# Kernel tuning notes

Hardware: AMD Instinct MI355X
Metric: run time of the kernel (lower is better)

The kernel has to match this reference:

```python
import jax, jax.numpy as jnp
import numpy as np

B, T, SD, CD = 2048, 512, 8, 8
H = 64 + SD  # control_rnn_size + state_dim = 72


def setup_inputs() -> dict:
    key = jax.random.key(0)
    ks = jax.random.split(key, 16)
    s = 0.05
    inp = {
        "x": jax.random.normal(ks[0], (B, SD), jnp.float32),
        "rnn_input": jax.random.normal(ks[1], (B, T, CD + 1), jnp.float32),
        "deltas": jax.random.uniform(ks[2], (B, T, 1), jnp.float32),
        "h_lens": jax.random.randint(ks[3], (B,), T // 2, T + 1, jnp.int32),
        "W_ih": s * jax.random.normal(ks[4], (4 * H, CD + 1), jnp.float32),
        "W_hh": s * jax.random.normal(ks[5], (4 * H, H), jnp.float32),
        "b_ih": jnp.zeros((4 * H,), jnp.float32),
        "b_hh": jnp.zeros((4 * H,), jnp.float32),
        "enc_W1": s * jax.random.normal(ks[6], (256, SD), jnp.float32),
        "enc_b1": jnp.zeros((256,), jnp.float32),
        "enc_W2": s * jax.random.normal(ks[7], (256, 256), jnp.float32),
        "enc_b2": jnp.zeros((256,), jnp.float32),
        "enc_W3": s * jax.random.normal(ks[8], (64, 256), jnp.float32),
        "enc_b3": jnp.zeros((64,), jnp.float32),
        "dec_W1": s * jax.random.normal(ks[9], (288, H), jnp.float32),
        "dec_b1": jnp.zeros((288,), jnp.float32),
        "dec_W2": s * jax.random.normal(ks[10], (288, 288), jnp.float32),
        "dec_b2": jnp.zeros((288,), jnp.float32),
        "dec_W3": s * jax.random.normal(ks[11], (SD, 288), jnp.float32),
        "dec_b3": jnp.zeros((SD,), jnp.float32),
    }
    return inp


def _mlp(z, Ws_bs):
    # Linear->Tanh repeated, final Linear without activation
    *hidden, (Wf, bf) = Ws_bs
    for W, b in hidden:
        z = jnp.tanh(z @ W.T + b)
    return z @ Wf.T + bf


def _lstm(rnn_input, h0, c0, W_ih, W_hh, b_ih, b_hh):
    # rnn_input: [B,T,I]; h0,c0: [B,H]. PyTorch gate order: i,f,g,o.
    x_proj = rnn_input @ W_ih.T + (b_ih + b_hh)  # [B,T,4H]

    def step(carry, xt):
        h, c = carry
        gates = xt + h @ W_hh.T
        i, f, g, o = jnp.split(gates, 4, axis=-1)
        i, f, o = jax.nn.sigmoid(i), jax.nn.sigmoid(f), jax.nn.sigmoid(o)
        c = f * c + i * jnp.tanh(g)
        h = o * jnp.tanh(c)
        return (h, c), h

    _, hs = jax.lax.scan(step, (h0, c0), jnp.swapaxes(x_proj, 0, 1))
    return jnp.swapaxes(hs, 0, 1)  # [B,T,H]


def reference(x, rnn_input, deltas, h_lens, W_ih, W_hh, b_ih, b_hh,
              enc_W1, enc_b1, enc_W2, enc_b2, enc_W3, enc_b3,
              dec_W1, dec_b1, dec_W2, dec_b2, dec_W3, dec_b3):
    h0 = _mlp(x, [(enc_W1, enc_b1), (enc_W2, enc_b2), (enc_W3, enc_b3)])  # [B,64]
    h0_stack = jnp.concatenate([x, h0], axis=1)  # [B,H]
    c0 = jnp.zeros_like(h0_stack)
    h = _lstm(rnn_input, h0_stack, c0, W_ih, W_hh, b_ih, b_hh)  # [B,T,H]
    # roll by 1 with h0 in slot 0
    h_shift = jnp.concatenate([h0_stack[:, None, :], h[:, :-1, :]], axis=1)
    encoded = (1.0 - deltas) * h_shift + deltas * h  # [B,T,H]
    dec_in = encoded[jnp.arange(encoded.shape[0]), h_lens - 1, :]  # [B,H]
    out = _mlp(dec_in, [(dec_W1, dec_b1), (dec_W2, dec_b2), (dec_W3, dec_b3)])
    return out[:, :SD]
```

## Files before the change

kernel.cpp:

```cpp
#include <hip/hip_runtime.h>
#include <cstdint>

#define HH 72
#define NR 8
#define NTH 576
#define NBLK 256
#define TT 512

typedef __attribute__((ext_vector_type(8))) _Float16 half8;
typedef __attribute__((ext_vector_type(4))) float f32x4;

#if __has_builtin(__builtin_amdgcn_exp2f)
#define EXP2(x) __builtin_amdgcn_exp2f(x)
#else
#define EXP2(x) exp2f(x)
#endif
#if __has_builtin(__builtin_amdgcn_rcpf)
#define RCP(x) __builtin_amdgcn_rcpf(x)
#else
#define RCP(x) (1.0f/(x))
#endif

__device__ __forceinline__ float fsig(float x) {
  float e = EXP2(x * -1.442695040888963f);
  return RCP(1.0f + e);
}
__device__ __forceinline__ float ftanh(float x) {
  float e = EXP2(x * -2.885390081777927f);
  return fmaf(2.0f, RCP(1.0f + e), -1.0f);
}

__device__ __forceinline__ unsigned short f2h(float v) {
  union { _Float16 h; unsigned short u; } cv;
  cv.h = (_Float16)v;
  return cv.u;
}

__device__ __forceinline__ int bidx(int k, int m) {
  return ((k >> 5)*4 + ((k >> 3) & 3))*64 + m*8 + (k & 7);
}

__device__ __forceinline__ float cellUpd(float ig, float fg, float gg, float og, float& c) {
  c = fmaf(fsig(fg), c, fsig(ig)*ftanh(gg));
  return fsig(og)*ftanh(c);
}

#define FMA4(A, W_, P_) { \
  const float4 _fa = *(const float4*)(P_); \
  A[0] = fmaf((W_), _fa.x, A[0]); A[1] = fmaf((W_), _fa.y, A[1]); \
  A[2] = fmaf((W_), _fa.z, A[2]); A[3] = fmaf((W_), _fa.w, A[3]); }

__global__ void cfm_sort(const int* __restrict__ h_lens, int* __restrict__ perm) {
  __shared__ int hist[257];
  __shared__ int offs[257];
  const int t = threadIdx.x;
  for (int i = t; i < 257; i += 256) hist[i] = 0;
  __syncthreads();
  for (int i = t; i < 2048; i += 256) {
    int bkt = min(max(h_lens[i] - 256, 0), 256);
    atomicAdd(&hist[bkt], 1);
  }
  __syncthreads();
  if (t == 0) { int s = 0; for (int i = 0; i < 257; ++i) { offs[i] = s; s += hist[i]; } }
  __syncthreads();
  for (int i = t; i < 2048; i += 256) {
    int bkt = min(max(h_lens[i] - 256, 0), 256);
    int pos = atomicAdd(&offs[bkt], 1);
    perm[pos] = i;
  }
}

__global__ __launch_bounds__(NTH, 2)
void cfm_main(const float* __restrict__ x, const float* __restrict__ rnn,
              const float* __restrict__ deltas, const int* __restrict__ h_lens,
              const float* __restrict__ W_ih, const float* __restrict__ W_hh,
              const float* __restrict__ b_ih, const float* __restrict__ b_hh,
              const float* __restrict__ eW1, const float* __restrict__ eb1,
              const float* __restrict__ eW2, const float* __restrict__ eb2,
              const float* __restrict__ eW3, const float* __restrict__ eb3,
              const float* __restrict__ dW1, const float* __restrict__ db1,
              const float* __restrict__ dW2, const float* __restrict__ db2,
              const float* __restrict__ dW3, const float* __restrict__ db3,
              const int* __restrict__ perm, float* __restrict__ out)
{
  __shared__ __align__(16) unsigned short hF[2][768];
  __shared__ __align__(16) float gS[2304];
  __shared__ __align__(16) float rnnS[2336];
  __shared__ __align__(16) float snapP[NR][HH];
  __shared__ __align__(16) float snapC[NR][HH];
  __shared__ __align__(16) float hS[HH*NR];
  __shared__ __align__(16) float xS[8*NR];
  __shared__ int brS[NR];
  __shared__ int idxS[NR];
  __shared__ float dS[NR];

  const int t  = threadIdx.x;
  const int bb = blockIdx.x;

  for (int i = t; i < 768; i += NTH) ((unsigned*)hF)[i] = 0;

  if (t < NR) {
    int row = perm ? perm[bb*NR + t] : (bb*NR + t);
    brS[t]  = row;
    idxS[t] = h_lens[row] - 1;
  }
  __syncthreads();

  int maxIdx = idxS[0];
  #pragma unroll
  for (int r = 1; r < NR; ++r) maxIdx = max(maxIdx, idxS[r]);

  const int lane = t & 63;
  const int wv   = t >> 6;
  const int col  = lane & 15;
  const int q_a  = lane >> 4;
  const int cL   = col & 7;
  const int gHi  = col >> 3;
  const int uA   = 4*(2*wv + gHi) + q_a;
  const int cidxE  = idxS[cL];
  const int cidxm1 = cidxE - 1;
  const int ibA  = bidx(uA, cL);
  const int bOff0 = (0*4 + q_a)*64 + cL*8;
  const int bOff1 = (1*4 + q_a)*64 + cL*8;
  const int bOff2 = (2*4 + q_a)*64 + cL*8;
  float cstA = 0.f;

  const int pfR = t / 72;
  const int pfP = t - pfR*72;
  const float4* rnnRow = (const float4*)(rnn + (size_t)brS[pfR]*4608) + pfP;
  float4 pf = rnnRow[0];

  const bool doXt = (t < 72);
  int xtDst = 0, xtSrc = 0;
  if (doXt) {
    int rX = t / 9, kX = t - rX*9;
    xtDst = bidx(72 + kX, rX);
    xtSrc = rX*292 + kX;
  }

  if (t < 64) { int r = t >> 3, k = t & 7; xS[k*8 + r] = x[brS[r]*8 + k]; }
  __syncthreads();

  float* z1S = gS;
  if (t < 512) {
    int n = t >> 1, rh = (t & 1)*4;
    float acc[4];
    float b = eb1[n];
    acc[0]=b; acc[1]=b; acc[2]=b; acc[3]=b;
    #pragma unroll
    for (int k = 0; k < 8; ++k) { float w = eW1[n*8 + k]; FMA4(acc, w, &xS[k*8 + rh]); }
    #pragma unroll
    for (int j = 0; j < 4; ++j) z1S[n*8 + rh + j] = ftanh(acc[j]);
  }
  __syncthreads();
  float* z2S = rnnS;
  if (t < 512) {
    int n = t >> 1, rh = (t & 1)*4;
    float acc[4];
    float b = eb2[n];
    acc[0]=b; acc[1]=b; acc[2]=b; acc[3]=b;
    const float4* w4 = (const float4*)(eW2 + n*256);
    #pragma unroll 4
    for (int k4 = 0; k4 < 64; ++k4) {
      float4 w = w4[k4];
      FMA4(acc, w.x, &z1S[(4*k4+0)*8 + rh]);
      FMA4(acc, w.y, &z1S[(4*k4+1)*8 + rh]);
      FMA4(acc, w.z, &z1S[(4*k4+2)*8 + rh]);
      FMA4(acc, w.w, &z1S[(4*k4+3)*8 + rh]);
    }
    #pragma unroll
    for (int j = 0; j < 4; ++j) z2S[n*8 + rh + j] = ftanh(acc[j]);
  }
  __syncthreads();
  if (t < 128) {
    int o = t >> 1, rh = (t & 1)*4;
    float acc[4];
    float b = eb3[o];
    acc[0]=b; acc[1]=b; acc[2]=b; acc[3]=b;
    const float4* w4 = (const float4*)(eW3 + o*256);
    #pragma unroll 4
    for (int k4 = 0; k4 < 64; ++k4) {
      float4 w = w4[k4];
      FMA4(acc, w.x, &z2S[(4*k4+0)*8 + rh]);
      FMA4(acc, w.y, &z2S[(4*k4+1)*8 + rh]);
      FMA4(acc, w.z, &z2S[(4*k4+2)*8 + rh]);
      FMA4(acc, w.w, &z2S[(4*k4+3)*8 + rh]);
    }
    #pragma unroll
    for (int j = 0; j < 4; ++j) hF[0][bidx(8 + o, rh + j)] = f2h(acc[j]);
  } else if (t < 192) {
    int tt2 = t - 128; int r = tt2 >> 3, k = tt2 & 7;
    hF[0][bidx(k, r)] = f2h(xS[k*8 + r]);
  }

  half8 Af[2][3];
  f32x4 biasq[2];
  #pragma unroll
  for (int i = 0; i < 2; ++i) {
    int u = 4*(2*wv + i) + q_a;
    biasq[i].x = b_ih[u]       + b_hh[u];
    biasq[i].y = b_ih[72 + u]  + b_hh[72 + u];
    biasq[i].z = b_ih[144 + u] + b_hh[144 + u];
    biasq[i].w = b_ih[216 + u] + b_hh[216 + u];
    int nprime = (2*wv + i)*16 + col;
    int srcrow = (nprime & 3)*72 + (nprime >> 2);
    #pragma unroll
    for (int kt = 0; kt < 3; ++kt) {
      union { unsigned short u16[8]; half8 h; } cw;
      #pragma unroll
      for (int j = 0; j < 8; ++j) {
        int k = kt*32 + q_a*8 + j;
        float v = 0.f;
        if (k < 72)      v = W_hh[srcrow*HH + k];
        else if (k < 81) v = W_ih[srcrow*9 + (k - 72)];
        cw.u16[j] = f2h(v);
      }
      Af[i][kt] = cw.h;
    }
  }

#define STEP(PAR) { \
    const unsigned short* hb = &hF[PAR][0]; \
    unsigned short* hn = &hF[(PAR) ^ 1][0]; \
    half8 bf0 = *(const half8*)(hb + bOff0); \
    half8 bf1 = *(const half8*)(hb + bOff1); \
    half8 bf2 = *(const half8*)(hb + bOff2); \
    f32x4 a0 = __builtin_amdgcn_mfma_f32_16x16x32_f16(Af[0][0], bf0, biasq[0], 0, 0, 0); \
    f32x4 a1 = __builtin_amdgcn_mfma_f32_16x16x32_f16(Af[1][0], bf0, biasq[1], 0, 0, 0); \
    a0 = __builtin_amdgcn_mfma_f32_16x16x32_f16(Af[0][1], bf1, a0, 0, 0, 0); \
    a1 = __builtin_amdgcn_mfma_f32_16x16x32_f16(Af[1][1], bf1, a1, 0, 0, 0); \
    a0 = __builtin_amdgcn_mfma_f32_16x16x32_f16(Af[0][2], bf2, a0, 0, 0, 0); \
    a1 = __builtin_amdgcn_mfma_f32_16x16x32_f16(Af[1][2], bf2, a1, 0, 0, 0); \
    float ig = gHi ? a1.x : a0.x; \
    float fg = gHi ? a1.y : a0.y; \
    float gg = gHi ? a1.z : a0.z; \
    float og = gHi ? a1.w : a0.w; \
    float hv = cellUpd(ig, fg, gg, og, cstA); \
    hn[ibA] = f2h(hv); \
    if (step == cidxm1) snapP[cL][uA] = hv; \
    if (step == cidxE)  snapC[cL][uA] = hv; \
    if (doXt && tc < 31) hn[xtDst] = f2h(rnnS[xtSrc + (tc + 1)*9]); \
    __syncthreads(); \
    ++tc; ++step; }

  int step = 0;
  for (int chunk = 0; chunk*32 <= maxIdx; ++chunk) {
    __syncthreads();
    *(float4*)&rnnS[pfR*292 + pfP*4] = pf;
    if ((chunk + 1)*32 <= maxIdx) pf = rnnRow[(chunk + 1)*72];
    __syncthreads();
    if (doXt) hF[0][xtDst] = f2h(rnnS[xtSrc]);
    __syncthreads();
    const int lim = min(31, maxIdx - chunk*32);
    int tc = 0;
    while (tc + 1 <= lim) { STEP(0) STEP(1) }
    if (tc <= lim) { STEP(0) }
  }
#undef STEP

  if (t < NR) dS[t] = deltas[brS[t]*TT + idxS[t]];
  __syncthreads();

  {
    int u = t % 72, r = t / 72;
    float d = dS[r];
    float sp = snapP[r][u], sc = snapC[r][u];
    hS[u*8 + r] = fmaf(d, sc - sp, sp);
  }
  __syncthreads();

  float* d1S = rnnS;
  {
    int n = t >> 1, rh = (t & 1)*4;
    float acc[4];
    float b = db1[n];
    acc[0]=b; acc[1]=b; acc[2]=b; acc[3]=b;
    const float4* w4 = (const float4*)(dW1 + n*HH);
    #pragma unroll 2
    for (int k4 = 0; k4 < 18; ++k4) {
      float4 w = w4[k4];
      FMA4(acc, w.x, &hS[(4*k4+0)*8 + rh]);
      FMA4(acc, w.y, &hS[(4*k4+1)*8 + rh]);
      FMA4(acc, w.z, &hS[(4*k4+2)*8 + rh]);
      FMA4(acc, w.w, &hS[(4*k4+3)*8 + rh]);
    }
    #pragma unroll
    for (int j = 0; j < 4; ++j) d1S[n*8 + rh + j] = ftanh(acc[j]);
  }
  __syncthreads();

  float* d2S = gS;
  {
    int n = t >> 1, rh = (t & 1)*4;
    float acc[4];
    float b = db2[n];
    acc[0]=b; acc[1]=b; acc[2]=b; acc[3]=b;
    const float4* w4 = (const float4*)(dW2 + n*288);
    #pragma unroll 4
    for (int k4 = 0; k4 < 72; ++k4) {
      float4 w = w4[k4];
      FMA4(acc, w.x, &d1S[(4*k4+0)*8 + rh]);
      FMA4(acc, w.y, &d1S[(4*k4+1)*8 + rh]);
      FMA4(acc, w.z, &d1S[(4*k4+2)*8 + rh]);
      FMA4(acc, w.w, &d1S[(4*k4+3)*8 + rh]);
    }
    #pragma unroll
    for (int j = 0; j < 4; ++j) d2S[n*8 + rh + j] = ftanh(acc[j]);
  }
  __syncthreads();

  if (t < 64) {
    int o = t & 7, r = t >> 3;
    float acc3 = db3[o];
    const float* wr = dW3 + o*288;
    #pragma unroll 4
    for (int k = 0; k < 288; ++k) acc3 = fmaf(wr[k], d2S[k*8 + r], acc3);
    out[brS[r]*8 + o] = acc3;
  }
}

extern "C" void kernel_launch(void* const* d_in, const int* in_sizes, int n_in,
                              void* d_out, int out_size, void* d_ws, size_t ws_size,
                              hipStream_t stream) {
  const float* x      = (const float*)d_in[0];
  const float* rnn    = (const float*)d_in[1];
  const float* deltas = (const float*)d_in[2];
  const int*   h_lens = (const int*)  d_in[3];
  const float* W_ih   = (const float*)d_in[4];
  const float* W_hh   = (const float*)d_in[5];
  const float* b_ih   = (const float*)d_in[6];
  const float* b_hh   = (const float*)d_in[7];
  const float* eW1    = (const float*)d_in[8];
  const float* eb1    = (const float*)d_in[9];
  const float* eW2    = (const float*)d_in[10];
  const float* eb2    = (const float*)d_in[11];
  const float* eW3    = (const float*)d_in[12];
  const float* eb3    = (const float*)d_in[13];
  const float* dW1    = (const float*)d_in[14];
  const float* db1    = (const float*)d_in[15];
  const float* dW2    = (const float*)d_in[16];
  const float* db2    = (const float*)d_in[17];
  const float* dW3    = (const float*)d_in[18];
  const float* db3    = (const float*)d_in[19];
  float* out = (float*)d_out;

  int* perm = nullptr;
  if (ws_size >= 2048 * sizeof(int)) {
    perm = (int*)d_ws;
    cfm_sort<<<1, 256, 0, stream>>>(h_lens, perm);
  }
  cfm_main<<<NBLK, NTH, 0, stream>>>(x, rnn, deltas, h_lens, W_ih, W_hh, b_ih, b_hh,
                                     eW1, eb1, eW2, eb2, eW3, eb3,
                                     dW1, db1, dW2, db2, dW3, db3,
                                     perm, out);
}
```

Measured before the change: 355.6 us.

## Process sixteen sequences per block with two interleaved MFMA groups

Each block now handles 16 batch rows as two 8-row groups, with half the blocks. Every recurrent step issues independent MFMA chains for both groups, so latency is hidden within one wave and the per-step barrier cost is shared across twice the rows. Snapshot captures move from conditional shared-memory stores into registers that are written once after the loop. The trade-offs are more shared memory and registers, only 128 blocks (fewer than the CU count), and a recurrence length set by the longer of 16 rows.

Result: slower. 524.9 us (+47.6%).

```diff
diff --git a/kernel.cpp b/kernel.cpp
--- a/kernel.cpp
+++ b/kernel.cpp
@@ -2,9 +2,9 @@
 #include <cstdint>
 
 #define HH 72
-#define NR 8
+#define NR 16
 #define NTH 576
-#define NBLK 256
+#define NBLK 128
 #define TT 512
 
 typedef __attribute__((ext_vector_type(8))) _Float16 half8;
@@ -45,10 +45,13 @@
   return fsig(og)*ftanh(c);
 }
 
-#define FMA4(A, W_, P_) { \
+#define FMA8(A, W_, P_) { \
   const float4 _fa = *(const float4*)(P_); \
+  const float4 _fb = *(const float4*)((P_) + 4); \
   A[0] = fmaf((W_), _fa.x, A[0]); A[1] = fmaf((W_), _fa.y, A[1]); \
-  A[2] = fmaf((W_), _fa.z, A[2]); A[3] = fmaf((W_), _fa.w, A[3]); }
+  A[2] = fmaf((W_), _fa.z, A[2]); A[3] = fmaf((W_), _fa.w, A[3]); \
+  A[4] = fmaf((W_), _fb.x, A[4]); A[5] = fmaf((W_), _fb.y, A[5]); \
+  A[6] = fmaf((W_), _fb.z, A[6]); A[7] = fmaf((W_), _fb.w, A[7]); }
 
 __global__ void cfm_sort(const int* __restrict__ h_lens, int* __restrict__ perm) {
   __shared__ int hist[257];
@@ -83,13 +86,13 @@
               const float* __restrict__ dW3, const float* __restrict__ db3,
               const int* __restrict__ perm, float* __restrict__ out)
 {
-  __shared__ __align__(16) unsigned short hF[2][768];
-  __shared__ __align__(16) float gS[2304];
-  __shared__ __align__(16) float rnnS[2336];
+  __shared__ __align__(16) unsigned short hF[2][2][768];
+  __shared__ __align__(16) float gS[4608];
+  __shared__ __align__(16) float rnnS[16*292];
   __shared__ __align__(16) float snapP[NR][HH];
   __shared__ __align__(16) float snapC[NR][HH];
-  __shared__ __align__(16) float hS[HH*NR];
-  __shared__ __align__(16) float xS[8*NR];
+  __shared__ __align__(16) float hS[HH*16];
+  __shared__ __align__(16) float xS[8*16];
   __shared__ int brS[NR];
   __shared__ int idxS[NR];
   __shared__ float dS[NR];
@@ -97,7 +100,7 @@
   const int t  = threadIdx.x;
   const int bb = blockIdx.x;
 
-  for (int i = t; i < 768; i += NTH) ((unsigned*)hF)[i] = 0;
+  for (int i = t; i < 1536; i += NTH) ((unsigned*)hF)[i] = 0;
 
   if (t < NR) {
     int row = perm ? perm[bb*NR + t] : (bb*NR + t);
@@ -117,80 +120,90 @@
   const int cL   = col & 7;
   const int gHi  = col >> 3;
   const int uA   = 4*(2*wv + gHi) + q_a;
-  const int cidxE  = idxS[cL];
-  const int cidxm1 = cidxE - 1;
+  const int cidxX   = idxS[cL];
+  const int cidxXm1 = cidxX - 1;
+  const int cidxY   = idxS[8 + cL];
+  const int cidxYm1 = cidxY - 1;
   const int ibA  = bidx(uA, cL);
   const int bOff0 = (0*4 + q_a)*64 + cL*8;
   const int bOff1 = (1*4 + q_a)*64 + cL*8;
   const int bOff2 = (2*4 + q_a)*64 + cL*8;
-  float cstA = 0.f;
+  float cstX = 0.f, cstY = 0.f;
+  float hvPX = 0.f, hvCX = 0.f, hvPY = 0.f, hvCY = 0.f;
 
   const int pfR = t / 72;
   const int pfP = t - pfR*72;
-  const float4* rnnRow = (const float4*)(rnn + (size_t)brS[pfR]*4608) + pfP;
-  float4 pf = rnnRow[0];
-
-  const bool doXt = (t < 72);
-  int xtDst = 0, xtSrc = 0;
+  const float4* rnnRowA = (const float4*)(rnn + (size_t)brS[pfR]*4608) + pfP;
+  const float4* rnnRowB = (const float4*)(rnn + (size_t)brS[pfR + 8]*4608) + pfP;
+  float4 pfA = rnnRowA[0];
+  float4 pfB = rnnRowB[0];
+
+  const bool doXt = (t < 144);
+  int xtDst = 0, xtSrc = 0, xtG = 0;
   if (doXt) {
     int rX = t / 9, kX = t - rX*9;
-    xtDst = bidx(72 + kX, rX);
+    xtG   = rX >> 3;
+    xtDst = bidx(72 + kX, rX & 7);
     xtSrc = rX*292 + kX;
   }
 
-  if (t < 64) { int r = t >> 3, k = t & 7; xS[k*8 + r] = x[brS[r]*8 + k]; }
+  if (t < 128) { int r = t >> 3, k = t & 7; xS[k*16 + r] = x[brS[r]*8 + k]; }
   __syncthreads();
 
   float* z1S = gS;
   if (t < 512) {
-    int n = t >> 1, rh = (t & 1)*4;
-    float acc[4];
+    int n = t >> 1, rh = (t & 1)*8;
+    float acc[8];
     float b = eb1[n];
-    acc[0]=b; acc[1]=b; acc[2]=b; acc[3]=b;
-    #pragma unroll
-    for (int k = 0; k < 8; ++k) { float w = eW1[n*8 + k]; FMA4(acc, w, &xS[k*8 + rh]); }
-    #pragma unroll
-    for (int j = 0; j < 4; ++j) z1S[n*8 + rh + j] = ftanh(acc[j]);
+    #pragma unroll
+    for (int j = 0; j < 8; ++j) acc[j] = b;
+    #pragma unroll
+    for (int k = 0; k < 8; ++k) { float w = eW1[n*8 + k]; FMA8(acc, w, &xS[k*16 + rh]); }
+    #pragma unroll
+    for (int j = 0; j < 8; ++j) z1S[n*16 + rh + j] = ftanh(acc[j]);
   }
   __syncthreads();
   float* z2S = rnnS;
   if (t < 512) {
-    int n = t >> 1, rh = (t & 1)*4;
-    float acc[4];
+    int n = t >> 1, rh = (t & 1)*8;
+    float acc[8];
     float b = eb2[n];
-    acc[0]=b; acc[1]=b; acc[2]=b; acc[3]=b;
+    #pragma unroll
+    for (int j = 0; j < 8; ++j) acc[j] = b;
     const float4* w4 = (const float4*)(eW2 + n*256);
-    #pragma unroll 4
+    #pragma unroll 2
     for (int k4 = 0; k4 < 64; ++k4) {
       float4 w = w4[k4];
-      FMA4(acc, w.x, &z1S[(4*k4+0)*8 + rh]);
-      FMA4(acc, w.y, &z1S[(4*k4+1)*8 + rh]);
-      FMA4(acc, w.z, &z1S[(4*k4+2)*8 + rh]);
-      FMA4(acc, w.w, &z1S[(4*k4+3)*8 + rh]);
-    }
-    #pragma unroll
-    for (int j = 0; j < 4; ++j) z2S[n*8 + rh + j] = ftanh(acc[j]);
+      FMA8(acc, w.x, &z1S[(4*k4+0)*16 + rh]);
+      FMA8(acc, w.y, &z1S[(4*k4+1)*16 + rh]);
+      FMA8(acc, w.z, &z1S[(4*k4+2)*16 + rh]);
+      FMA8(acc, w.w, &z1S[(4*k4+3)*16 + rh]);
+    }
+    #pragma unroll
+    for (int j = 0; j < 8; ++j) z2S[n*16 + rh + j] = ftanh(acc[j]);
   }
   __syncthreads();
   if (t < 128) {
-    int o = t >> 1, rh = (t & 1)*4;
-    float acc[4];
+    int o = t >> 1, rh = (t & 1)*8;
+    float acc[8];
     float b = eb3[o];
-    acc[0]=b; acc[1]=b; acc[2]=b; acc[3]=b;
+    #pragma unroll
+    for (int j = 0; j < 8; ++j) acc[j] = b;
     const float4* w4 = (const float4*)(eW3 + o*256);
-    #pragma unroll 4
+    #pragma unroll 2
     for (int k4 = 0; k4 < 64; ++k4) {
       float4 w = w4[k4];
-      FMA4(acc, w.x, &z2S[(4*k4+0)*8 + rh]);
-      FMA4(acc, w.y, &z2S[(4*k4+1)*8 + rh]);
-      FMA4(acc, w.z, &z2S[(4*k4+2)*8 + rh]);
-      FMA4(acc, w.w, &z2S[(4*k4+3)*8 + rh]);
-    }
-    #pragma unroll
-    for (int j = 0; j < 4; ++j) hF[0][bidx(8 + o, rh + j)] = f2h(acc[j]);
-  } else if (t < 192) {
+      FMA8(acc, w.x, &z2S[(4*k4+0)*16 + rh]);
+      FMA8(acc, w.y, &z2S[(4*k4+1)*16 + rh]);
+      FMA8(acc, w.z, &z2S[(4*k4+2)*16 + rh]);
+      FMA8(acc, w.w, &z2S[(4*k4+3)*16 + rh]);
+    }
+    int grp = rh >> 3;
+    #pragma unroll
+    for (int j = 0; j < 8; ++j) hF[grp][0][bidx(8 + o, j)] = f2h(acc[j]);
+  } else if (t < 256) {
     int tt2 = t - 128; int r = tt2 >> 3, k = tt2 & 7;
-    hF[0][bidx(k, r)] = f2h(xS[k*8 + r]);
+    hF[r >> 3][0][bidx(k, r & 7)] = f2h(xS[k*16 + r]);
   }
 
   half8 Af[2][3];
@@ -219,37 +232,53 @@
     }
   }
 
+#define MFMA16(A, B, C) __builtin_amdgcn_mfma_f32_16x16x32_f16(A, B, C, 0, 0, 0)
 #define STEP(PAR) { \
-    const unsigned short* hb = &hF[PAR][0]; \
-    unsigned short* hn = &hF[(PAR) ^ 1][0]; \
-    half8 bf0 = *(const half8*)(hb + bOff0); \
-    half8 bf1 = *(const half8*)(hb + bOff1); \
-    half8 bf2 = *(const half8*)(hb + bOff2); \
-    f32x4 a0 = __builtin_amdgcn_mfma_f32_16x16x32_f16(Af[0][0], bf0, biasq[0], 0, 0, 0); \
-    f32x4 a1 = __builtin_amdgcn_mfma_f32_16x16x32_f16(Af[1][0], bf0, biasq[1], 0, 0, 0); \
-    a0 = __builtin_amdgcn_mfma_f32_16x16x32_f16(Af[0][1], bf1, a0, 0, 0, 0); \
-    a1 = __builtin_amdgcn_mfma_f32_16x16x32_f16(Af[1][1], bf1, a1, 0, 0, 0); \
-    a0 = __builtin_amdgcn_mfma_f32_16x16x32_f16(Af[0][2], bf2, a0, 0, 0, 0); \
-    a1 = __builtin_amdgcn_mfma_f32_16x16x32_f16(Af[1][2], bf2, a1, 0, 0, 0); \
-    float ig = gHi ? a1.x : a0.x; \
-    float fg = gHi ? a1.y : a0.y; \
-    float gg = gHi ? a1.z : a0.z; \
-    float og = gHi ? a1.w : a0.w; \
-    float hv = cellUpd(ig, fg, gg, og, cstA); \
-    hn[ibA] = f2h(hv); \
-    if (step == cidxm1) snapP[cL][uA] = hv; \
-    if (step == cidxE)  snapC[cL][uA] = hv; \
-    if (doXt && tc < 31) hn[xtDst] = f2h(rnnS[xtSrc + (tc + 1)*9]); \
+    const unsigned short* hbX = &hF[0][PAR][0]; \
+    const unsigned short* hbY = &hF[1][PAR][0]; \
+    unsigned short* hnX = &hF[0][(PAR) ^ 1][0]; \
+    unsigned short* hnY = &hF[1][(PAR) ^ 1][0]; \
+    half8 bx0 = *(const half8*)(hbX + bOff0); \
+    half8 bx1 = *(const half8*)(hbX + bOff1); \
+    half8 bx2 = *(const half8*)(hbX + bOff2); \
+    half8 by0 = *(const half8*)(hbY + bOff0); \
+    half8 by1 = *(const half8*)(hbY + bOff1); \
+    half8 by2 = *(const half8*)(hbY + bOff2); \
+    f32x4 ax0 = MFMA16(Af[0][0], bx0, biasq[0]); \
+    f32x4 ax1 = MFMA16(Af[1][0], bx0, biasq[1]); \
+    f32x4 ay0 = MFMA16(Af[0][0], by0, biasq[0]); \
+    f32x4 ay1 = MFMA16(Af[1][0], by0, biasq[1]); \
+    ax0 = MFMA16(Af[0][1], bx1, ax0);  ax1 = MFMA16(Af[1][1], bx1, ax1); \
+    ay0 = MFMA16(Af[0][1], by1, ay0);  ay1 = MFMA16(Af[1][1], by1, ay1); \
+    ax0 = MFMA16(Af[0][2], bx2, ax0);  ax1 = MFMA16(Af[1][2], bx2, ax1); \
+    ay0 = MFMA16(Af[0][2], by2, ay0);  ay1 = MFMA16(Af[1][2], by2, ay1); \
+    float igX = gHi ? ax1.x : ax0.x, fgX = gHi ? ax1.y : ax0.y; \
+    float ggX = gHi ? ax1.z : ax0.z, ogX = gHi ? ax1.w : ax0.w; \
+    float igY = gHi ? ay1.x : ay0.x, fgY = gHi ? ay1.y : ay0.y; \
+    float ggY = gHi ? ay1.z : ay0.z, ogY = gHi ? ay1.w : ay0.w; \
+    float hvX = cellUpd(igX, fgX, ggX, ogX, cstX); \
+    float hvY = cellUpd(igY, fgY, ggY, ogY, cstY); \
+    hnX[ibA] = f2h(hvX); \
+    hnY[ibA] = f2h(hvY); \
+    hvPX = (step == cidxXm1) ? hvX : hvPX; \
+    hvCX = (step == cidxX)   ? hvX : hvCX; \
+    hvPY = (step == cidxYm1) ? hvY : hvPY; \
+    hvCY = (step == cidxY)   ? hvY : hvCY; \
+    if (doXt && tc < 31) (xtG ? hnY : hnX)[xtDst] = f2h(rnnS[xtSrc + (tc + 1)*9]); \
     __syncthreads(); \
     ++tc; ++step; }
 
   int step = 0;
   for (int chunk = 0; chunk*32 <= maxIdx; ++chunk) {
     __syncthreads();
-    *(float4*)&rnnS[pfR*292 + pfP*4] = pf;
-    if ((chunk + 1)*32 <= maxIdx) pf = rnnRow[(chunk + 1)*72];
+    *(float4*)&rnnS[pfR*292 + pfP*4] = pfA;
+    *(float4*)&rnnS[(pfR + 8)*292 + pfP*4] = pfB;
+    if ((chunk + 1)*32 <= maxIdx) {
+      pfA = rnnRowA[(chunk + 1)*72];
+      pfB = rnnRowB[(chunk + 1)*72];
+    }
     __syncthreads();
-    if (doXt) hF[0][xtDst] = f2h(rnnS[xtSrc]);
+    if (doXt) hF[xtG][0][xtDst] = f2h(rnnS[xtSrc]);
     __syncthreads();
     const int lim = min(31, maxIdx - chunk*32);
     int tc = 0;
@@ -257,64 +286,69 @@
     if (tc <= lim) { STEP(0) }
   }
 #undef STEP
-
+#undef MFMA16
+
+  snapP[cL][uA]     = hvPX;  snapC[cL][uA]     = hvCX;
+  snapP[8 + cL][uA] = hvPY;  snapC[8 + cL][uA] = hvCY;
   if (t < NR) dS[t] = deltas[brS[t]*TT + idxS[t]];
   __syncthreads();
 
-  {
-    int u = t % 72, r = t / 72;
+  for (int p = t; p < HH*16; p += NTH) {
+    int u = p >> 4, r = p & 15;
     float d = dS[r];
     float sp = snapP[r][u], sc = snapC[r][u];
-    hS[u*8 + r] = fmaf(d, sc - sp, sp);
+    hS[u*16 + r] = fmaf(d, sc - sp, sp);
   }
   __syncthreads();
 
   float* d1S = rnnS;
   {
-    int n = t >> 1, rh = (t & 1)*4;
-    float acc[4];
+    int n = t >> 1, rh = (t & 1)*8;
+    float acc[8];
     float b = db1[n];
-    acc[0]=b; acc[1]=b; acc[2]=b; acc[3]=b;
+    #pragma unroll
+    for (int j = 0; j < 8; ++j) acc[j] = b;
     const float4* w4 = (const float4*)(dW1 + n*HH);
     #pragma unroll 2
     for (int k4 = 0; k4 < 18; ++k4) {
       float4 w = w4[k4];
-      FMA4(acc, w.x, &hS[(4*k4+0)*8 + rh]);
-      FMA4(acc, w.y, &hS[(4*k4+1)*8 + rh]);
-      FMA4(acc, w.z, &hS[(4*k4+2)*8 + rh]);
-      FMA4(acc, w.w, &hS[(4*k4+3)*8 + rh]);
-    }
-    #pragma unroll
-    for (int j = 0; j < 4; ++j) d1S[n*8 + rh + j] = ftanh(acc[j]);
+      FMA8(acc, w.x, &hS[(4*k4+0)*16 + rh]);
+      FMA8(acc, w.y, &hS[(4*k4+1)*16 + rh]);
+      FMA8(acc, w.z, &hS[(4*k4+2)*16 + rh]);
+      FMA8(acc, w.w, &hS[(4*k4+3)*16 + rh]);
+    }
+    #pragma unroll
+    for (int j = 0; j < 8; ++j) d1S[n*16 + rh + j] = ftanh(acc[j]);
   }
   __syncthreads();
 
   float* d2S = gS;
   {
-    int n = t >> 1, rh = (t & 1)*4;
-    float acc[4];
+    int n = t >> 1, rh = (t & 1)*8;
+    float acc[8];
     float b = db2[n];
-    acc[0]=b; acc[1]=b; acc[2]=b; acc[3]=b;
+    #pragma unroll
+    for (int j = 0; j < 8; ++j) acc[j] = b;
     const float4* w4 = (const float4*)(dW2 + n*288);
-    #pragma unroll 4
+    #pragma unroll 2
     for (int k4 = 0; k4 < 72; ++k4) {
       float4 w = w4[k4];
-      FMA4(acc, w.x, &d1S[(4*k4+0)*8 + rh]);
-      FMA4(acc, w.y, &d1S[(4*k4+1)*8 + rh]);
-      FMA4(acc, w.z, &d1S[(4*k4+2)*8 + rh]);
-      FMA4(acc, w.w, &d1S[(4*k4+3)*8 + rh]);
-    }
-    #pragma unroll
-    for (int j = 0; j < 4; ++j) d2S[n*8 + rh + j] = ftanh(acc[j]);
-  }
-  __syncthreads();
-
-  if (t < 64) {
+      FMA8(acc, w.x, &d1S[(4*k4+0)*16 + rh]);
+      FMA8(acc, w.y, &d1S[(4*k4+1)*16 + rh]);
+      FMA8(acc, w.z, &d1S[(4*k4+2)*16 + rh]);
+      FMA8(acc, w.w, &d1S[(4*k4+3)*16 + rh]);
+    }
+    #pragma unroll
+    for (int j = 0; j < 8; ++j) d2S[n*16 + rh + j] = ftanh(acc[j]);
+  }
+  __syncthreads();
+
+  if (t < 128) {
     int o = t & 7, r = t >> 3;
     float acc3 = db3[o];
     const float* wr = dW3 + o*288;
     #pragma unroll 4
-    for (int k = 0; k < 288; ++k) acc3 = fmaf(wr[k], d2S[k*8 + r], acc3);
+    for (int k = 0; k < 288; ++k) acc3 = fmaf(wr[k], d2S[k*16 + r], acc3);
     out[brS[r]*8 + o] = acc3;
   }
 }
```

## Shrink LSTM block to three waves, each computing six gate tiles per step

Applied to the files above, without the earlier changes.

Cuts the block from 576 to 192 threads, so each wave issues 18 MFMAs per timestep over six 16-row gate tiles and updates three cell states per lane. The aim is to make the per-step __syncthreads cheaper by having fewer waves join the barrier, and to give each wave independent MFMA chains that hide latency. Snapshot hidden states are now held in registers and written out once after the loop, replacing per-step conditional shared stores. In exchange each wave does three times the serial work per step, register pressure rises with 18 A fragments, and the MLP stages now loop over fewer threads.

Result: slower. 445.1 us (+25.2%).

```diff
diff --git a/kernel.cpp b/kernel.cpp
--- a/kernel.cpp
+++ b/kernel.cpp
@@ -3,7 +3,7 @@
 
 #define HH 72
 #define NR 8
-#define NTH 576
+#define NTH 192
 #define NBLK 256
 #define TT 512
 
@@ -70,7 +70,7 @@
   }
 }
 
-__global__ __launch_bounds__(NTH, 2)
+__global__ __launch_bounds__(NTH, 1)
 void cfm_main(const float* __restrict__ x, const float* __restrict__ rnn,
               const float* __restrict__ deltas, const int* __restrict__ h_lens,
               const float* __restrict__ W_ih, const float* __restrict__ W_hh,
@@ -116,19 +116,28 @@
   const int q_a  = lane >> 4;
   const int cL   = col & 7;
   const int gHi  = col >> 3;
-  const int uA   = 4*(2*wv + gHi) + q_a;
+  const int tb   = 6*wv + 3*gHi;
+  const int uA0  = 4*(tb + 0) + q_a;
+  const int uA1  = 4*(tb + 1) + q_a;
+  const int uA2  = 4*(tb + 2) + q_a;
+  const int ib0  = bidx(uA0, cL);
+  const int ib1  = bidx(uA1, cL);
+  const int ib2  = bidx(uA2, cL);
   const int cidxE  = idxS[cL];
   const int cidxm1 = cidxE - 1;
-  const int ibA  = bidx(uA, cL);
   const int bOff0 = (0*4 + q_a)*64 + cL*8;
   const int bOff1 = (1*4 + q_a)*64 + cL*8;
   const int bOff2 = (2*4 + q_a)*64 + cL*8;
-  float cstA = 0.f;
-
-  const int pfR = t / 72;
-  const int pfP = t - pfR*72;
-  const float4* rnnRow = (const float4*)(rnn + (size_t)brS[pfR]*4608) + pfP;
-  float4 pf = rnnRow[0];
+  float cst0 = 0.f, cst1 = 0.f, cst2 = 0.f;
+  float hP0 = 0.f, hP1 = 0.f, hP2 = 0.f;
+  float hC0 = 0.f, hC1 = 0.f, hC2 = 0.f;
+
+  const int pfR = t / 24;
+  const int pfC = t - pfR*24;
+  const float4* rnnRow = (const float4*)(rnn + (size_t)brS[pfR]*4608) + pfC*3;
+  float4 pf0 = rnnRow[0];
+  float4 pf1 = rnnRow[1];
+  float4 pf2 = rnnRow[2];
 
   const bool doXt = (t < 72);
   int xtDst = 0, xtSrc = 0;
@@ -142,8 +151,8 @@
   __syncthreads();
 
   float* z1S = gS;
-  if (t < 512) {
-    int n = t >> 1, rh = (t & 1)*4;
+  for (int p = t; p < 512; p += NTH) {
+    int n = p >> 1, rh = (p & 1)*4;
     float acc[4];
     float b = eb1[n];
     acc[0]=b; acc[1]=b; acc[2]=b; acc[3]=b;
@@ -154,8 +163,8 @@
   }
   __syncthreads();
   float* z2S = rnnS;
-  if (t < 512) {
-    int n = t >> 1, rh = (t & 1)*4;
+  for (int p = t; p < 512; p += NTH) {
+    int n = p >> 1, rh = (p & 1)*4;
     float acc[4];
     float b = eb2[n];
     acc[0]=b; acc[1]=b; acc[2]=b; acc[3]=b;
@@ -188,21 +197,21 @@
     }
     #pragma unroll
     for (int j = 0; j < 4; ++j) hF[0][bidx(8 + o, rh + j)] = f2h(acc[j]);
-  } else if (t < 192) {
+  } else {
     int tt2 = t - 128; int r = tt2 >> 3, k = tt2 & 7;
     hF[0][bidx(k, r)] = f2h(xS[k*8 + r]);
   }
 
-  half8 Af[2][3];
-  f32x4 biasq[2];
+  half8 Af[6][3];
+  f32x4 biasq[6];
   #pragma unroll
-  for (int i = 0; i < 2; ++i) {
-    int u = 4*(2*wv + i) + q_a;
+  for (int i = 0; i < 6; ++i) {
+    int u = 4*(6*wv + i) + q_a;
     biasq[i].x = b_ih[u]       + b_hh[u];
     biasq[i].y = b_ih[72 + u]  + b_hh[72 + u];
     biasq[i].z = b_ih[144 + u] + b_hh[144 + u];
     biasq[i].w = b_ih[216 + u] + b_hh[216 + u];
-    int nprime = (2*wv + i)*16 + col;
+    int nprime = (6*wv + i)*16 + col;
     int srcrow = (nprime & 3)*72 + (nprime >> 2);
     #pragma unroll
     for (int kt = 0; kt < 3; ++kt) {
@@ -219,26 +228,40 @@
     }
   }
 
+#define MFMA16(A, B, C) __builtin_amdgcn_mfma_f32_16x16x32_f16(A, B, C, 0, 0, 0)
 #define STEP(PAR) { \
     const unsigned short* hb = &hF[PAR][0]; \
     unsigned short* hn = &hF[(PAR) ^ 1][0]; \
     half8 bf0 = *(const half8*)(hb + bOff0); \
     half8 bf1 = *(const half8*)(hb + bOff1); \
     half8 bf2 = *(const half8*)(hb + bOff2); \
-    f32x4 a0 = __builtin_amdgcn_mfma_f32_16x16x32_f16(Af[0][0], bf0, biasq[0], 0, 0, 0); \
-    f32x4 a1 = __builtin_amdgcn_mfma_f32_16x16x32_f16(Af[1][0], bf0, biasq[1], 0, 0, 0); \
-    a0 = __builtin_amdgcn_mfma_f32_16x16x32_f16(Af[0][1], bf1, a0, 0, 0, 0); \
-    a1 = __builtin_amdgcn_mfma_f32_16x16x32_f16(Af[1][1], bf1, a1, 0, 0, 0); \
-    a0 = __builtin_amdgcn_mfma_f32_16x16x32_f16(Af[0][2], bf2, a0, 0, 0, 0); \
-    a1 = __builtin_amdgcn_mfma_f32_16x16x32_f16(Af[1][2], bf2, a1, 0, 0, 0); \
-    float ig = gHi ? a1.x : a0.x; \
-    float fg = gHi ? a1.y : a0.y; \
-    float gg = gHi ? a1.z : a0.z; \
-    float og = gHi ? a1.w : a0.w; \
-    float hv = cellUpd(ig, fg, gg, og, cstA); \
-    hn[ibA] = f2h(hv); \
-    if (step == cidxm1) snapP[cL][uA] = hv; \
-    if (step == cidxE)  snapC[cL][uA] = hv; \
+    f32x4 a0 = MFMA16(Af[0][0], bf0, biasq[0]); \
+    f32x4 a1 = MFMA16(Af[1][0], bf0, biasq[1]); \
+    f32x4 a2 = MFMA16(Af[2][0], bf0, biasq[2]); \
+    f32x4 a3 = MFMA16(Af[3][0], bf0, biasq[3]); \
+    f32x4 a4 = MFMA16(Af[4][0], bf0, biasq[4]); \
+    f32x4 a5 = MFMA16(Af[5][0], bf0, biasq[5]); \
+    a0 = MFMA16(Af[0][1], bf1, a0);  a1 = MFMA16(Af[1][1], bf1, a1); \
+    a2 = MFMA16(Af[2][1], bf1, a2);  a3 = MFMA16(Af[3][1], bf1, a3); \
+    a4 = MFMA16(Af[4][1], bf1, a4);  a5 = MFMA16(Af[5][1], bf1, a5); \
+    a0 = MFMA16(Af[0][2], bf2, a0);  a1 = MFMA16(Af[1][2], bf2, a1); \
+    a2 = MFMA16(Af[2][2], bf2, a2);  a3 = MFMA16(Af[3][2], bf2, a3); \
+    a4 = MFMA16(Af[4][2], bf2, a4);  a5 = MFMA16(Af[5][2], bf2, a5); \
+    float i0 = gHi ? a3.x : a0.x, f0 = gHi ? a3.y : a0.y; \
+    float g0 = gHi ? a3.z : a0.z, o0 = gHi ? a3.w : a0.w; \
+    float i1 = gHi ? a4.x : a1.x, f1 = gHi ? a4.y : a1.y; \
+    float g1 = gHi ? a4.z : a1.z, o1 = gHi ? a4.w : a1.w; \
+    float i2 = gHi ? a5.x : a2.x, f2 = gHi ? a5.y : a2.y; \
+    float g2 = gHi ? a5.z : a2.z, o2 = gHi ? a5.w : a2.w; \
+    float hv0 = cellUpd(i0, f0, g0, o0, cst0); \
+    float hv1 = cellUpd(i1, f1, g1, o1, cst1); \
+    float hv2 = cellUpd(i2, f2, g2, o2, cst2); \
+    hn[ib0] = f2h(hv0); \
+    hn[ib1] = f2h(hv1); \
+    hn[ib2] = f2h(hv2); \
+    hP0 = (step == cidxm1) ? hv0 : hP0;  hC0 = (step == cidxE) ? hv0 : hC0; \
+    hP1 = (step == cidxm1) ? hv1 : hP1;  hC1 = (step == cidxE) ? hv1 : hC1; \
+    hP2 = (step == cidxm1) ? hv2 : hP2;  hC2 = (step == cidxE) ? hv2 : hC2; \
     if (doXt && tc < 31) hn[xtDst] = f2h(rnnS[xtSrc + (tc + 1)*9]); \
     __syncthreads(); \
     ++tc; ++step; }
@@ -246,8 +269,14 @@
   int step = 0;
   for (int chunk = 0; chunk*32 <= maxIdx; ++chunk) {
     __syncthreads();
-    *(float4*)&rnnS[pfR*292 + pfP*4] = pf;
-    if ((chunk + 1)*32 <= maxIdx) pf = rnnRow[(chunk + 1)*72];
+    *(float4*)&rnnS[pfR*292 + pfC*12 + 0] = pf0;
+    *(float4*)&rnnS[pfR*292 + pfC*12 + 4] = pf1;
+    *(float4*)&rnnS[pfR*292 + pfC*12 + 8] = pf2;
+    if ((chunk + 1)*32 <= maxIdx) {
+      pf0 = rnnRow[(chunk + 1)*72 + 0];
+      pf1 = rnnRow[(chunk + 1)*72 + 1];
+      pf2 = rnnRow[(chunk + 1)*72 + 2];
+    }
     __syncthreads();
     if (doXt) hF[0][xtDst] = f2h(rnnS[xtSrc]);
     __syncthreads();
@@ -257,12 +286,16 @@
     if (tc <= lim) { STEP(0) }
   }
 #undef STEP
-
+#undef MFMA16
+
+  snapP[cL][uA0] = hP0;  snapC[cL][uA0] = hC0;
+  snapP[cL][uA1] = hP1;  snapC[cL][uA1] = hC1;
+  snapP[cL][uA2] = hP2;  snapC[cL][uA2] = hC2;
   if (t < NR) dS[t] = deltas[brS[t]*TT + idxS[t]];
   __syncthreads();
 
-  {
-    int u = t % 72, r = t / 72;
+  for (int p = t; p < HH*NR; p += NTH) {
+    int u = p >> 3, r = p & 7;
     float d = dS[r];
     float sp = snapP[r][u], sc = snapC[r][u];
     hS[u*8 + r] = fmaf(d, sc - sp, sp);
@@ -270,8 +303,8 @@
   __syncthreads();
 
   float* d1S = rnnS;
-  {
-    int n = t >> 1, rh = (t & 1)*4;
+  for (int p = t; p < 576; p += NTH) {
+    int n = p >> 1, rh = (p & 1)*4;
     float acc[4];
     float b = db1[n];
     acc[0]=b; acc[1]=b; acc[2]=b; acc[3]=b;
@@ -290,8 +323,8 @@
   __syncthreads();
 
   float* d2S = gS;
-  {
-    int n = t >> 1, rh = (t & 1)*4;
+  for (int p = t; p < 576; p += NTH) {
+    int n = p >> 1, rh = (p & 1)*4;
     float acc[4];
     float b = db2[n];
     acc[0]=b; acc[1]=b; acc[2]=b; acc[3]=b;
```

## Halve rows per block to double block count and overlap recurrences per CU

Applied to the files above, without the earlier changes.

Each block now processes 4 batch rows instead of 8, and the launch uses 512 blocks instead of 256. Launch bounds allow 4 blocks per CU, so two latency-bound LSTM recurrences can interleave on one CU. Sorted groups are assigned to blocks in an interleaved order to even out sequence lengths across the two halves of the grid. Final-step snapshots are kept in registers and written to shared memory once after the loop, instead of being stored conditionally at every step. The cost is that the 16-column MFMA tiles are now only a quarter used, and every block repeats the weight loads and encoder work.

Result: slower. 574.2 us (+61.5%).

```diff
diff --git a/kernel.cpp b/kernel.cpp
--- a/kernel.cpp
+++ b/kernel.cpp
@@ -2,9 +2,9 @@
 #include <cstdint>
 
 #define HH 72
-#define NR 8
+#define NR 4
 #define NTH 576
-#define NBLK 256
+#define NBLK 512
 #define TT 512
 
 typedef __attribute__((ext_vector_type(8))) _Float16 half8;
@@ -37,7 +37,7 @@
 }
 
 __device__ __forceinline__ int bidx(int k, int m) {
-  return ((k >> 5)*4 + ((k >> 3) & 3))*64 + m*8 + (k & 7);
+  return ((k >> 5)*4 + ((k >> 3) & 3))*32 + m*8 + (k & 7);
 }
 
 __device__ __forceinline__ float cellUpd(float ig, float fg, float gg, float og, float& c) {
@@ -45,10 +45,9 @@
   return fsig(og)*ftanh(c);
 }
 
-#define FMA4(A, W_, P_) { \
-  const float4 _fa = *(const float4*)(P_); \
-  A[0] = fmaf((W_), _fa.x, A[0]); A[1] = fmaf((W_), _fa.y, A[1]); \
-  A[2] = fmaf((W_), _fa.z, A[2]); A[3] = fmaf((W_), _fa.w, A[3]); }
+#define FMA2(A, W_, P_) { \
+  const float2 _fa = *(const float2*)(P_); \
+  A[0] = fmaf((W_), _fa.x, A[0]); A[1] = fmaf((W_), _fa.y, A[1]); }
 
 __global__ void cfm_sort(const int* __restrict__ h_lens, int* __restrict__ perm) {
   __shared__ int hist[257];
@@ -70,7 +69,7 @@
   }
 }
 
-__global__ __launch_bounds__(NTH, 2)
+__global__ __launch_bounds__(NTH, 4)
 void cfm_main(const float* __restrict__ x, const float* __restrict__ rnn,
               const float* __restrict__ deltas, const int* __restrict__ h_lens,
               const float* __restrict__ W_ih, const float* __restrict__ W_hh,
@@ -83,9 +82,9 @@
               const float* __restrict__ dW3, const float* __restrict__ db3,
               const int* __restrict__ perm, float* __restrict__ out)
 {
-  __shared__ __align__(16) unsigned short hF[2][768];
-  __shared__ __align__(16) float gS[2304];
-  __shared__ __align__(16) float rnnS[2336];
+  __shared__ __align__(16) unsigned short hF[2][384];
+  __shared__ __align__(16) float gS[1152];
+  __shared__ __align__(16) float rnnS[1168];
   __shared__ __align__(16) float snapP[NR][HH];
   __shared__ __align__(16) float snapC[NR][HH];
   __shared__ __align__(16) float hS[HH*NR];
@@ -96,11 +95,12 @@
 
   const int t  = threadIdx.x;
   const int bb = blockIdx.x;
-
-  for (int i = t; i < 768; i += NTH) ((unsigned*)hF)[i] = 0;
+  const int pgrp = (bb < 256) ? (2*bb) : (2*(bb - 256) + 1);
+
+  for (int i = t; i < 384; i += NTH) ((unsigned*)hF)[i] = 0;
 
   if (t < NR) {
-    int row = perm ? perm[bb*NR + t] : (bb*NR + t);
+    int row = perm ? perm[pgrp*NR + t] : (pgrp*NR + t);
     brS[t]  = row;
     idxS[t] = h_lens[row] - 1;
   }
@@ -114,23 +114,26 @@
   const int wv   = t >> 6;
   const int col  = lane & 15;
   const int q_a  = lane >> 4;
-  const int cL   = col & 7;
+  const int cL   = col & 3;
   const int gHi  = col >> 3;
   const int uA   = 4*(2*wv + gHi) + q_a;
   const int cidxE  = idxS[cL];
   const int cidxm1 = cidxE - 1;
   const int ibA  = bidx(uA, cL);
-  const int bOff0 = (0*4 + q_a)*64 + cL*8;
-  const int bOff1 = (1*4 + q_a)*64 + cL*8;
-  const int bOff2 = (2*4 + q_a)*64 + cL*8;
+  const int bOff0 = (0*4 + q_a)*32 + cL*8;
+  const int bOff1 = (1*4 + q_a)*32 + cL*8;
+  const int bOff2 = (2*4 + q_a)*32 + cL*8;
   float cstA = 0.f;
+  float hvP = 0.f, hvC = 0.f;
 
   const int pfR = t / 72;
   const int pfP = t - pfR*72;
-  const float4* rnnRow = (const float4*)(rnn + (size_t)brS[pfR]*4608) + pfP;
-  float4 pf = rnnRow[0];
-
-  const bool doXt = (t < 72);
+  const bool doPf = (t < 288);
+  const float4* rnnRow = doPf ? ((const float4*)(rnn + (size_t)brS[pfR]*4608) + pfP)
+                              : (const float4*)rnn;
+  float4 pf = doPf ? rnnRow[0] : float4{0,0,0,0};
+
+  const bool doXt = (t < 36);
   int xtDst = 0, xtSrc = 0;
   if (doXt) {
     int rX = t / 9, kX = t - rX*9;
@@ -138,59 +141,59 @@
     xtSrc = rX*292 + kX;
   }
 
-  if (t < 64) { int r = t >> 3, k = t & 7; xS[k*8 + r] = x[brS[r]*8 + k]; }
+  if (t < 32) { int r = t >> 3, k = t & 7; xS[k*4 + r] = x[brS[r]*8 + k]; }
   __syncthreads();
 
   float* z1S = gS;
   if (t < 512) {
-    int n = t >> 1, rh = (t & 1)*4;
-    float acc[4];
+    int n = t >> 1, rh = (t & 1)*2;
+    float acc[2];
     float b = eb1[n];
-    acc[0]=b; acc[1]=b; acc[2]=b; acc[3]=b;
-    #pragma unroll
-    for (int k = 0; k < 8; ++k) { float w = eW1[n*8 + k]; FMA4(acc, w, &xS[k*8 + rh]); }
-    #pragma unroll
-    for (int j = 0; j < 4; ++j) z1S[n*8 + rh + j] = ftanh(acc[j]);
+    acc[0]=b; acc[1]=b;
+    #pragma unroll
+    for (int k = 0; k < 8; ++k) { float w = eW1[n*8 + k]; FMA2(acc, w, &xS[k*4 + rh]); }
+    #pragma unroll
+    for (int j = 0; j < 2; ++j) z1S[n*4 + rh + j] = ftanh(acc[j]);
   }
   __syncthreads();
   float* z2S = rnnS;
   if (t < 512) {
-    int n = t >> 1, rh = (t & 1)*4;
-    float acc[4];
+    int n = t >> 1, rh = (t & 1)*2;
+    float acc[2];
     float b = eb2[n];
-    acc[0]=b; acc[1]=b; acc[2]=b; acc[3]=b;
+    acc[0]=b; acc[1]=b;
     const float4* w4 = (const float4*)(eW2 + n*256);
     #pragma unroll 4
     for (int k4 = 0; k4 < 64; ++k4) {
       float4 w = w4[k4];
-      FMA4(acc, w.x, &z1S[(4*k4+0)*8 + rh]);
-      FMA4(acc, w.y, &z1S[(4*k4+1)*8 + rh]);
-      FMA4(acc, w.z, &z1S[(4*k4+2)*8 + rh]);
-      FMA4(acc, w.w, &z1S[(4*k4+3)*8 + rh]);
-    }
-    #pragma unroll
-    for (int j = 0; j < 4; ++j) z2S[n*8 + rh + j] = ftanh(acc[j]);
+      FMA2(acc, w.x, &z1S[(4*k4+0)*4 + rh]);
+      FMA2(acc, w.y, &z1S[(4*k4+1)*4 + rh]);
+      FMA2(acc, w.z, &z1S[(4*k4+2)*4 + rh]);
+      FMA2(acc, w.w, &z1S[(4*k4+3)*4 + rh]);
+    }
+    #pragma unroll
+    for (int j = 0; j < 2; ++j) z2S[n*4 + rh + j] = ftanh(acc[j]);
   }
   __syncthreads();
   if (t < 128) {
-    int o = t >> 1, rh = (t & 1)*4;
-    float acc[4];
+    int o = t >> 1, rh = (t & 1)*2;
+    float acc[2];
     float b = eb3[o];
-    acc[0]=b; acc[1]=b; acc[2]=b; acc[3]=b;
+    acc[0]=b; acc[1]=b;
     const float4* w4 = (const float4*)(eW3 + o*256);
     #pragma unroll 4
     for (int k4 = 0; k4 < 64; ++k4) {
       float4 w = w4[k4];
-      FMA4(acc, w.x, &z2S[(4*k4+0)*8 + rh]);
-      FMA4(acc, w.y, &z2S[(4*k4+1)*8 + rh]);
-      FMA4(acc, w.z, &z2S[(4*k4+2)*8 + rh]);
-      FMA4(acc, w.w, &z2S[(4*k4+3)*8 + rh]);
-    }
-    #pragma unroll
-    for (int j = 0; j < 4; ++j) hF[0][bidx(8 + o, rh + j)] = f2h(acc[j]);
-  } else if (t < 192) {
+      FMA2(acc, w.x, &z2S[(4*k4+0)*4 + rh]);
+      FMA2(acc, w.y, &z2S[(4*k4+1)*4 + rh]);
+      FMA2(acc, w.z, &z2S[(4*k4+2)*4 + rh]);
+      FMA2(acc, w.w, &z2S[(4*k4+3)*4 + rh]);
+    }
+    #pragma unroll
+    for (int j = 0; j < 2; ++j) hF[0][bidx(8 + o, rh + j)] = f2h(acc[j]);
+  } else if (t < 160) {
     int tt2 = t - 128; int r = tt2 >> 3, k = tt2 & 7;
-    hF[0][bidx(k, r)] = f2h(xS[k*8 + r]);
+    hF[0][bidx(k, r)] = f2h(xS[k*4 + r]);
   }
 
   half8 Af[2][3];
@@ -219,26 +222,23 @@
     }
   }
 
+#define MFMA16(A, B, C) __builtin_amdgcn_mfma_f32_16x16x32_f16(A, B, C, 0, 0, 0)
 #define STEP(PAR) { \
     const unsigned short* hb = &hF[PAR][0]; \
     unsigned short* hn = &hF[(PAR) ^ 1][0]; \
     half8 bf0 = *(const half8*)(hb + bOff0); \
     half8 bf1 = *(const half8*)(hb + bOff1); \
     half8 bf2 = *(const half8*)(hb + bOff2); \
-    f32x4 a0 = __builtin_amdgcn_mfma_f32_16x16x32_f16(Af[0][0], bf0, biasq[0], 0, 0, 0); \
-    f32x4 a1 = __builtin_amdgcn_mfma_f32_16x16x32_f16(Af[1][0], bf0, biasq[1], 0, 0, 0); \
-    a0 = __builtin_amdgcn_mfma_f32_16x16x32_f16(Af[0][1], bf1, a0, 0, 0, 0); \
-    a1 = __builtin_amdgcn_mfma_f32_16x16x32_f16(Af[1][1], bf1, a1, 0, 0, 0); \
-    a0 = __builtin_amdgcn_mfma_f32_16x16x32_f16(Af[0][2], bf2, a0, 0, 0, 0); \
-    a1 = __builtin_amdgcn_mfma_f32_16x16x32_f16(Af[1][2], bf2, a1, 0, 0, 0); \
-    float ig = gHi ? a1.x : a0.x; \
-    float fg = gHi ? a1.y : a0.y; \
-    float gg = gHi ? a1.z : a0.z; \
-    float og = gHi ? a1.w : a0.w; \
+    f32x4 a0 = MFMA16(Af[0][0], bf0, biasq[0]); \
+    f32x4 a1 = MFMA16(Af[1][0], bf0, biasq[1]); \
+    a0 = MFMA16(Af[0][1], bf1, a0);  a1 = MFMA16(Af[1][1], bf1, a1); \
+    a0 = MFMA16(Af[0][2], bf2, a0);  a1 = MFMA16(Af[1][2], bf2, a1); \
+    float ig = gHi ? a1.x : a0.x, fg = gHi ? a1.y : a0.y; \
+    float gg = gHi ? a1.z : a0.z, og = gHi ? a1.w : a0.w; \
     float hv = cellUpd(ig, fg, gg, og, cstA); \
     hn[ibA] = f2h(hv); \
-    if (step == cidxm1) snapP[cL][uA] = hv; \
-    if (step == cidxE)  snapC[cL][uA] = hv; \
+    hvP = (step == cidxm1) ? hv : hvP; \
+    hvC = (step == cidxE)  ? hv : hvC; \
     if (doXt && tc < 31) hn[xtDst] = f2h(rnnS[xtSrc + (tc + 1)*9]); \
     __syncthreads(); \
     ++tc; ++step; }
@@ -246,8 +246,8 @@
   int step = 0;
   for (int chunk = 0; chunk*32 <= maxIdx; ++chunk) {
     __syncthreads();
-    *(float4*)&rnnS[pfR*292 + pfP*4] = pf;
-    if ((chunk + 1)*32 <= maxIdx) pf = rnnRow[(chunk + 1)*72];
+    if (doPf) *(float4*)&rnnS[pfR*292 + pfP*4] = pf;
+    if (doPf && (chunk + 1)*32 <= maxIdx) pf = rnnRow[(chunk + 1)*72];
     __syncthreads();
     if (doXt) hF[0][xtDst] = f2h(rnnS[xtSrc]);
     __syncthreads();
@@ -257,64 +257,66 @@
     if (tc <= lim) { STEP(0) }
   }
 #undef STEP
-
+#undef MFMA16
+
+  snapP[cL][uA] = hvP;  snapC[cL][uA] = hvC;
   if (t < NR) dS[t] = deltas[brS[t]*TT + idxS[t]];
   __syncthreads();
 
-  {
-    int u = t % 72, r = t / 72;
+  if (t < HH*NR) {
+    int u = t >> 2, r = t & 3;
     float d = dS[r];
     float sp = snapP[r][u], sc = snapC[r][u];
-    hS[u*8 + r] = fmaf(d, sc - sp, sp);
+    hS[u*4 + r] = fmaf(d, sc - sp, sp);
   }
   __syncthreads();
 
   float* d1S = rnnS;
   {
-    int n = t >> 1, rh = (t & 1)*4;
-    float acc[4];
+    int n = t >> 1, rh = (t & 1)*2;
+    float acc[2];
     float b = db1[n];
-    acc[0]=b; acc[1]=b; acc[2]=b; acc[3]=b;
+    acc[0]=b; acc[1]=b;
     const float4* w4 = (const float4*)(dW1 + n*HH);
     #pragma unroll 2
     for (int k4 = 0; k4 < 18; ++k4) {
       float4 w = w4[k4];
-      FMA4(acc, w.x, &hS[(4*k4+0)*8 + rh]);
-      FMA4(acc, w.y, &hS[(4*k4+1)*8 + rh]);
-      FMA4(acc, w.z, &hS[(4*k4+2)*8 + rh]);
-      FMA4(acc, w.w, &hS[(4*k4+3)*8 + rh]);
-    }
-    #pragma unroll
-    for (int j = 0; j < 4; ++j) d1S[n*8 + rh + j] = ftanh(acc[j]);
+      FMA2(acc, w.x, &hS[(4*k4+0)*4 + rh]);
+      FMA2(acc, w.y, &hS[(4*k4+1)*4 + rh]);
+      FMA2(acc, w.z, &hS[(4*k4+2)*4 + rh]);
+      FMA2(acc, w.w, &hS[(4*k4+3)*4 + rh]);
+    }
+    #pragma unroll
+    for (int j = 0; j < 2; ++j) d1S[n*4 + rh + j] = ftanh(acc[j]);
   }
   __syncthreads();
 
   float* d2S = gS;
   {
-    int n = t >> 1, rh = (t & 1)*4;
-    float acc[4];
+    int n = t >> 1, rh = (t & 1)*2;
+    float acc[2];
     float b = db2[n];
-    acc[0]=b; acc[1]=b; acc[2]=b; acc[3]=b;
+    acc[0]=b; acc[1]=b;
     const float4* w4 = (const float4*)(dW2 + n*288);
     #pragma unroll 4
     for (int k4 = 0; k4 < 72; ++k4) {
       float4 w = w4[k4];
-      FMA4(acc, w.x, &d1S[(4*k4+0)*8 + rh]);
-      FMA4(acc, w.y, &d1S[(4*k4+1)*8 + rh]);
-      FMA4(acc, w.z, &d1S[(4*k4+2)*8 + rh]);
-      FMA4(acc, w.w, &d1S[(4*k4+3)*8 + rh]);
-    }
-    #pragma unroll
-    for (int j = 0; j < 4; ++j) d2S[n*8 + rh + j] = ftanh(acc[j]);
-  }
-  __syncthreads();
-
-  if (t < 64) {
+      FMA2(acc, w.x, &d1S[(4*k4+0)*4 + rh]);
+      FMA2(acc, w.y, &d1S[(4*k4+1)*4 + rh]);
+      FMA2(acc, w.z, &d1S[(4*k4+2)*4 + rh]);
+      FMA2(acc, w.w, &d1S[(4*k4+3)*4 + rh]);
+    }
+    #pragma unroll
+    for (int j = 0; j < 2; ++j) d2S[n*4 + rh + j] = ftanh(acc[j]);
+  }
+  __syncthreads();
+
+  if (t < 32) {
     int o = t & 7, r = t >> 3;
     float acc3 = db3[o];
     const float* wr = dW3 + o*288;
     #pragma unroll 4
-    for (int k = 0; k < 288; ++k) acc3 = fmaf(wr[k], d2S[k*8 + r], acc3);
+    for (int k = 0; k < 288; ++k) acc3 = fmaf(wr[k], d2S[k*4 + r], acc3);
     out[brS[r]*8 + o] = acc3;
   }
 }
```
